# Kernel tuning notes

Measured on AMD Instinct MI355X. Metric: run time of the kernel, lower is better.

The kernel has to match this reference:

```python
import jax, jax.numpy as jnp
import numpy as np

T = 8
TAU = 2.0       # spikingjelly LIFNode default tau
VTH = 1.0       # default v_threshold
ALPHA = 2.0     # surrogate.ATan alpha
EPS = 1e-5      # BatchNorm eps


@jax.custom_vjp
def spike_fn(x):
    # Heaviside with ATan surrogate gradient
    return (x >= 0.0).astype(x.dtype)

def _spike_fwd(x):
    return (x >= 0.0).astype(x.dtype), x

def _spike_bwd(x, g):
    sg = (ALPHA / 2.0) / (1.0 + (jnp.pi / 2.0 * ALPHA * x) ** 2)
    return (g * sg,)

spike_fn.defvjp(_spike_fwd, _spike_bwd)


def lif(x_seq):
    """Multi-step LIF over leading time axis. decay_input=True, hard reset to 0, detach_reset."""
    def step(v, x):
        v = v + (x - v) / TAU            # charge
        s = spike_fn(v - VTH)            # fire (surrogate grad)
        v = v * (1.0 - jax.lax.stop_gradient(s))  # detached hard reset to v_reset=0
        return v, s
    _, s_seq = jax.lax.scan(step, jnp.zeros_like(x_seq[0]), x_seq)
    return s_seq


def conv2d(x, w, b, stride):
    y = jax.lax.conv_general_dilated(x, w, (stride, stride), 'VALID',
                                     dimension_numbers=('NCHW', 'OIHW', 'NCHW'))
    return y + b[None, :, None, None]


def batchnorm(x, g, b):
    # training-mode BN over merged (T*B, H, W) axes, matching step_mode='m' BatchNorm2d
    m = x.mean((0, 2, 3), keepdims=True)
    v = x.var((0, 2, 3), keepdims=True)
    return g[None, :, None, None] * (x - m) * jax.lax.rsqrt(v + EPS) + b[None, :, None, None]


def setup_inputs() -> dict:
    key = jax.random.key(0)
    ks = jax.random.split(key, 12)
    def w_init(k, shape):
        fan_in = int(np.prod(shape[1:]))
        return jax.random.normal(k, shape, dtype=jnp.float32) / np.sqrt(fan_in)
    x = jax.random.normal(ks[0], (128, 4, 84, 84), dtype=jnp.float32)
    return {
        'x': x,
        'conv1_w': w_init(ks[1], (32, 4, 8, 8)),  'conv1_b': jnp.zeros((32,), jnp.float32),
        'bn1_g': jnp.ones((32,), jnp.float32),    'bn1_b': jnp.zeros((32,), jnp.float32),
        'conv2_w': w_init(ks[2], (64, 32, 4, 4)), 'conv2_b': jnp.zeros((64,), jnp.float32),
        'bn2_g': jnp.ones((64,), jnp.float32),    'bn2_b': jnp.zeros((64,), jnp.float32),
        'conv3_w': w_init(ks[3], (64, 64, 3, 3)), 'conv3_b': jnp.zeros((64,), jnp.float32),
        'bn3_g': jnp.ones((64,), jnp.float32),    'bn3_b': jnp.zeros((64,), jnp.float32),
        'fc1_w': w_init(ks[4], (512, 3136)),      'fc1_b': jnp.zeros((512,), jnp.float32),
        'fco_w': w_init(ks[5], (2, 512)),         'fco_b': jnp.zeros((2,), jnp.float32),
    }


def reference(x, conv1_w, conv1_b, bn1_g, bn1_b, conv2_w, conv2_b, bn2_g, bn2_b,
              conv3_w, conv3_b, bn3_g, bn3_b, fc1_w, fc1_b, fco_w, fco_b):
    B = x.shape[0]
    # replicate input over T timesteps; fold T into batch for conv/BN (step_mode='m')
    xs = jnp.broadcast_to(x, (T,) + x.shape).reshape((T * B,) + x.shape[1:])

    h = batchnorm(conv2d(xs, conv1_w, conv1_b, 4), bn1_g, bn1_b)   # [TB,32,20,20]
    s = lif(h.reshape((T, B) + h.shape[1:]))
    h = s.reshape((T * B,) + s.shape[2:])

    h = batchnorm(conv2d(h, conv2_w, conv2_b, 2), bn2_g, bn2_b)    # [TB,64,9,9]
    s = lif(h.reshape((T, B) + h.shape[1:]))
    h = s.reshape((T * B,) + s.shape[2:])

    h = batchnorm(conv2d(h, conv3_w, conv3_b, 1), bn3_g, bn3_b)    # [TB,64,7,7]
    s = lif(h.reshape((T, B) + h.shape[1:]))                        # [T,B,64,7,7]

    feat = s.reshape(T, B, -1)                                      # [T,B,3136]
    hid = lif(jnp.einsum('tbi,oi->tbo', feat, fc1_w) + fc1_b)       # [T,B,512]
    out_seq = jnp.einsum('tbo,ko->tbk', hid, fco_w) + fco_b         # [T,B,2]
    return out_seq.mean(0)                                          # [B,2]
```

## Files before the change

kernel.cpp:

```cpp
#include <hip/hip_runtime.h>
#include <cstdint>
#include <cstddef>

#define TT 8

#define H1_ELEMS (128*32*20*20)
#define E2_ELEMS (128*64*81)
#define E3_ELEMS (128*64*49)

typedef __attribute__((ext_vector_type(8))) short short8;
typedef __attribute__((ext_vector_type(4))) float f32x4;

__global__ void prep_wT1(const float* __restrict__ w1, float* __restrict__ wT1) {
  int i = blockIdx.x * 256 + threadIdx.x;
  if (i >= 8192) return;
  int oc = i >> 8, pos = i & 255;
  wT1[(oc >> 4) * 4096 + pos * 16 + (oc & 15)] = w1[oc * 256 + pos];
}

__global__ void prep_w2frag(const float* __restrict__ w2, __bf16* __restrict__ wf) {
  int i = blockIdx.x * 256 + threadIdx.x;
  if (i >= 98304) return;
  int j    = i & 7;
  int oc   = (i >> 3) & 63;
  int quad = (i >> 9) & 3;
  int ksg  = (i >> 11) & 15;
  int term = i >> 15;
  int k = ksg * 32 + quad * 8 + j;
  int ci = k >> 4, kpos = k & 15;
  float w = w2[oc * 512 + ci * 16 + kpos];
  float hf = (float)(__bf16)w;
  float r1 = w - hf;
  float mf = (float)(__bf16)r1;
  float r2 = r1 - mf;
  __bf16 val = (term == 0) ? (__bf16)w : (term == 1) ? (__bf16)r1 : (__bf16)r2;
  wf[i] = val;
}

__global__ void prep_w3frag(const float* __restrict__ w3, __bf16* __restrict__ wf) {
  int i = blockIdx.x * 256 + threadIdx.x;
  if (i >= 110592) return;
  int j    = i & 7;
  int oc   = (i >> 3) & 63;
  int quad = (i >> 9) & 3;
  int tk   = i >> 11;
  int term = tk / 18, kstep = tk % 18;
  int k = kstep * 32 + quad * 8 + j;
  int pos = k >> 6, ci = k & 63;
  float w = w3[oc * 576 + ci * 9 + pos];
  float hf = (float)(__bf16)w;
  float r1 = w - hf;
  float mf = (float)(__bf16)r1;
  float r2 = r1 - mf;
  __bf16 val = (term == 0) ? (__bf16)w : (term == 1) ? (__bf16)r1 : (__bf16)r2;
  wf[i] = val;
}

__global__ void prep_wTf(const float* __restrict__ w, float* __restrict__ wT) {
  __shared__ float tile[32][33];
  int k0 = blockIdx.x * 32;
  int o0 = blockIdx.y * 32;
  int tx = threadIdx.x & 31, ty = threadIdx.x >> 5;
  #pragma unroll
  for (int j = 0; j < 4; j++)
    tile[ty + j * 8][tx] = w[(size_t)(o0 + ty + j * 8) * 3136 + k0 + tx];
  __syncthreads();
  #pragma unroll
  for (int j = 0; j < 4; j++)
    wT[(size_t)(k0 + ty + j * 8) * 512 + o0 + tx] = tile[tx][ty + j * 8];
}

__global__ __launch_bounds__(128) void k_conv1(const float* __restrict__ x,
                                               const float* __restrict__ wT,
                                               const float* __restrict__ bias,
                                               float* __restrict__ out) {
  __shared__ float xt[8064];
  int tid = threadIdx.x;
  int img = blockIdx.x >> 2;
  int q   = blockIdx.x & 3;
  int och = blockIdx.y;
  float4* dst = (float4*)xt;
  #pragma unroll
  for (int ci = 0; ci < 4; ci++) {
    const float4* s4 = (const float4*)(x + (size_t)img * 28224 + ci * 7056 + q * 1680);
    for (int i = tid; i < 504; i += 128) dst[ci * 504 + i] = s4[i];
  }
  __syncthreads();
  if (tid >= 100) return;
  int oyl = tid / 20, ox = tid % 20;
  float acc[16];
  #pragma unroll
  for (int j = 0; j < 16; j++) acc[j] = 0.f;
  int xb0 = oyl * 336 + ox * 4;
  const float* wh = wT + och * 4096;
  #pragma unroll 1
  for (int ci = 0; ci < 4; ci++) {
    #pragma unroll 1
    for (int ky = 0; ky < 8; ky++) {
      const float* xr = xt + ci * 2016 + xb0 + ky * 84;
      float4 xa  = *(const float4*)xr;
      float4 xbv = *(const float4*)(xr + 4);
      const float* wr = wh + (ci * 8 + ky) * 128;
      float xs[8] = {xa.x, xa.y, xa.z, xa.w, xbv.x, xbv.y, xbv.z, xbv.w};
      #pragma unroll
      for (int kx = 0; kx < 8; kx++) {
        #pragma unroll
        for (int j = 0; j < 16; j++)
          acc[j] = fmaf(xs[kx], wr[kx * 16 + j], acc[j]);
      }
    }
  }
  size_t obase = (size_t)img * 12800 + och * 6400 + (q * 5 + oyl) * 20 + ox;
  #pragma unroll
  for (int j = 0; j < 16; j++) out[obase + j * 400] = acc[j] + bias[och * 16 + j];
}

template <int HW>
__global__ void k_bnpartial(const float* __restrict__ xp, int C, int Nper,
                            float* __restrict__ pout) {
  int c = blockIdx.x, s = blockIdx.y, S = gridDim.y, tid = threadIdx.x;
  int n = Nper * HW;
  float sum = 0.f, sum2 = 0.f;
  for (int i = tid; i < n; i += 256) {
    int nb = s * Nper + i / HW;
    int p  = i % HW;
    float v = xp[((size_t)nb * C + c) * HW + p];
    sum += v; sum2 += v * v;
  }
  __shared__ float l0[256], l1[256];
  l0[tid] = sum; l1[tid] = sum2; __syncthreads();
  for (int k = 128; k > 0; k >>= 1) {
    if (tid < k) { l0[tid] += l0[tid + k]; l1[tid] += l1[tid + k]; }
    __syncthreads();
  }
  if (tid == 0) { pout[(c * S + s) * 2] = l0[0]; pout[(c * S + s) * 2 + 1] = l1[0]; }
}

__global__ void k_bnfinal(const float* __restrict__ pin, int S, float n,
                          float* __restrict__ meanArr, float* __restrict__ rstdArr) {
  int c = blockIdx.x, lane = threadIdx.x;
  float s = 0.f, s2 = 0.f;
  if (lane < S) { s = pin[(c * S + lane) * 2]; s2 = pin[(c * S + lane) * 2 + 1]; }
  for (int off = 8; off > 0; off >>= 1) { s += __shfl_down(s, off); s2 += __shfl_down(s2, off); }
  if (lane == 0) {
    float m = s / n;
    float var = s2 / n - m * m;
    meanArr[c] = m;
    rstdArr[c] = rsqrtf(var + 1e-5f);
  }
}

__global__ void k_lif1b(const float* __restrict__ h, const float* __restrict__ mean,
                        const float* __restrict__ rstd, const float* __restrict__ g,
                        const float* __restrict__ bb, uint32_t* __restrict__ sout) {
  int idx = blockIdx.x * 256 + threadIdx.x;
  int ic = idx / 20;
  int ci = ic & 31;
  const float* hp = h + (size_t)idx * 20;
  float gm = g[ci], mm = mean[ci], rs = rstd[ci], bc = bb[ci];
  float xv[20];
  #pragma unroll
  for (int j4 = 0; j4 < 5; j4++) {
    float4 hv = ((const float4*)hp)[j4];
    xv[j4 * 4 + 0] = gm * (hv.x - mm) * rs + bc;
    xv[j4 * 4 + 1] = gm * (hv.y - mm) * rs + bc;
    xv[j4 * 4 + 2] = gm * (hv.z - mm) * rs + bc;
    xv[j4 * 4 + 3] = gm * (hv.w - mm) * rs + bc;
  }
  float v[20];
  #pragma unroll
  for (int j = 0; j < 20; j++) v[j] = 0.f;
  #pragma unroll
  for (int t = 0; t < TT; t++) {
    uint32_t w = 0;
    #pragma unroll
    for (int j = 0; j < 20; j++) {
      v[j] = v[j] + (xv[j] - v[j]) * 0.5f;
      uint32_t s = (v[j] >= 1.0f);
      w |= s << j;
      if (s) v[j] = 0.f;
    }
    sout[t * 81920 + idx] = w;
  }
}

template <int W, int NROW>
__global__ void k_lifb(const float* __restrict__ h, const float* __restrict__ mean,
                       const float* __restrict__ rstd, const float* __restrict__ g,
                       const float* __restrict__ bb, uint32_t* __restrict__ sout,
                       int E) {
  int idx = blockIdx.x * 256 + threadIdx.x;
  int bc = idx / NROW;
  int c = bc & 63;
  float gm = g[c], mm = mean[c], rs = rstd[c], bcn = bb[c];
  float v[W];
  #pragma unroll
  for (int j = 0; j < W; j++) v[j] = 0.f;
  int nword = 128 * 64 * NROW;
  #pragma unroll
  for (int t = 0; t < TT; t++) {
    const float* hp = h + (size_t)t * E + (size_t)idx * W;
    uint32_t w = 0;
    #pragma unroll
    for (int j = 0; j < W; j++) {
      float xv = gm * (hp[j] - mm) * rs + bcn;
      v[j] = v[j] + (xv - v[j]) * 0.5f;
      uint32_t s = (v[j] >= 1.0f);
      w |= s << j;
      if (s) v[j] = 0.f;
    }
    sout[t * nword + idx] = w;
  }
}

__global__ __launch_bounds__(256) void k_conv2m(const uint32_t* __restrict__ s1b,
                                                const __bf16* __restrict__ wf,
                                                const float* __restrict__ bias,
                                                float* __restrict__ out) {
  __shared__ uint32_t sp[1280];
  __shared__ uint4 wl4[3072];
  __bf16* wl = (__bf16*)wl4;
  int tid = threadIdx.x;
  int img0 = blockIdx.x * 2;
  {
    const uint32_t* src = s1b + (size_t)img0 * 640;
    for (int i = tid; i < 1280; i += 256) sp[i] = src[i];
  }
  int wave = tid >> 6, lane = tid & 63;
  int img_local = wave >> 1;
  int tg = wave & 1;
  int l15 = lane & 15, quad = lane >> 4;
  int ci_off = quad >> 1;
  int kyp = (quad & 1) * 2;
  int spb[3], sh[3];
  #pragma unroll
  for (int mt = 0; mt < 3; mt++) {
    int px = tg * 48 + mt * 16 + l15;
    if (px > 80) px = 80;
    int oy = px / 9, ox = px - oy * 9;
    sh[mt]  = ox * 2;
    spb[mt] = img_local * 640 + ci_off * 20 + oy * 2 + kyp;
  }
  f32x4 acc[3][4];
  #pragma unroll
  for (int mt = 0; mt < 3; mt++)
    #pragma unroll
    for (int nt = 0; nt < 4; nt++) acc[mt][nt] = (f32x4){0.f, 0.f, 0.f, 0.f};

  for (int kc = 0; kc < 4; kc++) {
    __syncthreads();
    for (int o = tid * 8; o < 24576; o += 2048) {
      int tk = o >> 11;
      int term = tk >> 2, ksl = tk & 3;
      const __bf16* src = wf + (((term * 16 + kc * 4 + ksl)) << 11) + (o & 2047);
      *(uint4*)(wl + o) = *(const uint4*)src;
    }
    __syncthreads();
    #pragma unroll
    for (int ks = 0; ks < 4; ks++) {
      int ksg = kc * 4 + ks;
      short8 a[3];
      #pragma unroll
      for (int mt = 0; mt < 3; mt++) {
        uint32_t w0 = sp[spb[mt] + ksg * 40];
        uint32_t w1 = sp[spb[mt] + ksg * 40 + 1];
        uint32_t n0 = (w0 >> sh[mt]) & 15u;
        uint32_t n1 = (w1 >> sh[mt]) & 15u;
        union { uint32_t u[4]; short8 v; } A;
        A.u[0] = ((n0 & 1u) ? 0x3F80u : 0u) | ((n0 & 2u) ? 0x3F800000u : 0u);
        A.u[1] = ((n0 & 4u) ? 0x3F80u : 0u) | ((n0 & 8u) ? 0x3F800000u : 0u);
        A.u[2] = ((n1 & 1u) ? 0x3F80u : 0u) | ((n1 & 2u) ? 0x3F800000u : 0u);
        A.u[3] = ((n1 & 4u) ? 0x3F80u : 0u) | ((n1 & 8u) ? 0x3F800000u : 0u);
        a[mt] = A.v;
      }
      #pragma unroll
      for (int term = 0; term < 3; term++) {
        int fb = ((term * 4 + ks) << 11) + (quad << 9);
        #pragma unroll
        for (int nt = 0; nt < 4; nt++) {
          short8 b = *(const short8*)(wl + fb + ((nt << 4) + l15) * 8);
          #pragma unroll
          for (int mt = 0; mt < 3; mt++)
            acc[mt][nt] = __builtin_amdgcn_mfma_f32_16x16x32_bf16(a[mt], b, acc[mt][nt], 0, 0, 0);
        }
      }
    }
  }
  #pragma unroll
  for (int nt = 0; nt < 4; nt++) {
    int oc = nt * 16 + l15;
    float bv = bias[oc];
    float* op = out + ((size_t)(img0 + img_local) * 64 + oc) * 81;
    #pragma unroll
    for (int mt = 0; mt < 3; mt++) {
      int pxr = tg * 48 + mt * 16 + quad * 4;
      #pragma unroll
      for (int r = 0; r < 4; r++) {
        int px = pxr + r;
        if (px < 81) op[px] = acc[mt][nt][r] + bv;
      }
    }
  }
}

__global__ void k_s2T(const uint32_t* __restrict__ sbits, uint32_t* __restrict__ s2T) {
  __shared__ uint32_t sb[576];
  int n = blockIdx.x;
  int t = n >> 7, b = n & 127;
  int tid = threadIdx.x;
  const uint32_t* src = sbits + t * 73728 + b * 576;
  for (int i = tid; i < 576; i += 256) sb[i] = src[i];
  __syncthreads();
  if (tid >= 162) return;
  int half = tid & 1, pc = tid >> 1;
  int r = pc / 9, cpix = pc - r * 9;
  uint32_t w = 0;
  #pragma unroll
  for (int ci = 0; ci < 32; ci++)
    w |= (((sb[(half * 32 + ci) * 9 + r] >> cpix) & 1u) << ci);
  s2T[(size_t)n * 162 + pc * 2 + half] = w;
}

__global__ __launch_bounds__(256) void k_conv3m(const uint32_t* __restrict__ s2T,
                                                const __bf16* __restrict__ wf,
                                                const float* __restrict__ bias,
                                                float* __restrict__ out) {
  __shared__ uint32_t sp[324];
  __shared__ uint4 wl4[4608];
  __bf16* wl = (__bf16*)wl4;
  int tid = threadIdx.x;
  int img0 = blockIdx.x * 2;
  {
    const uint32_t* src = s2T + (size_t)img0 * 162;
    for (int i = tid; i < 324; i += 256) sp[i] = src[i];
  }
  int wave = tid >> 6, lane = tid & 63;
  int img_local = wave >> 1, tg = wave & 1;
  int l15 = lane & 15, quad = lane >> 4;
  int qsh = quad * 8;
  int base[2];
  #pragma unroll
  for (int mt = 0; mt < 2; mt++) {
    int px = tg * 32 + mt * 16 + l15;
    if (px > 48) px = 48;
    int oy = px / 7, ox = px - oy * 7;
    base[mt] = img_local * 162 + (oy * 9 + ox) * 2;
  }
  f32x4 acc[2][4];
  #pragma unroll
  for (int mt = 0; mt < 2; mt++)
    #pragma unroll
    for (int nt = 0; nt < 4; nt++) acc[mt][nt] = (f32x4){0.f, 0.f, 0.f, 0.f};

  #pragma unroll
  for (int kc = 0; kc < 3; kc++) {
    __syncthreads();
    #pragma unroll
    for (int it = 0; it < 18; it++) {
      const __bf16* s = wf + (((it / 6) * 18 + kc * 6 + (it % 6)) << 11) + tid * 8;
      *(uint4*)(wl + (it << 11) + tid * 8) = *(const uint4*)s;
    }
    __syncthreads();
    #pragma unroll
    for (int ksl = 0; ksl < 6; ksl++) {
      int kstep = kc * 6 + ksl;
      int pos = kstep >> 1, cihalf = kstep & 1;
      int ky = pos / 3, kx = pos % 3;
      short8 a[2];
      #pragma unroll
      for (int mt = 0; mt < 2; mt++) {
        uint32_t word = sp[base[mt] + (ky * 9 + kx) * 2 + cihalf];
        uint32_t byt = (word >> qsh) & 255u;
        union { uint32_t u[4]; short8 v; } A;
        A.u[0] = ((byt & 1u)  ? 0x3F80u : 0u) | ((byt & 2u)   ? 0x3F800000u : 0u);
        A.u[1] = ((byt & 4u)  ? 0x3F80u : 0u) | ((byt & 8u)   ? 0x3F800000u : 0u);
        A.u[2] = ((byt & 16u) ? 0x3F80u : 0u) | ((byt & 32u)  ? 0x3F800000u : 0u);
        A.u[3] = ((byt & 64u) ? 0x3F80u : 0u) | ((byt & 128u) ? 0x3F800000u : 0u);
        a[mt] = A.v;
      }
      #pragma unroll
      for (int term = 0; term < 3; term++) {
        int fb = ((term * 6 + ksl) << 11) + (quad << 9);
        #pragma unroll
        for (int nt = 0; nt < 4; nt++) {
          short8 b = *(const short8*)(wl + fb + ((nt << 4) + l15) * 8);
          #pragma unroll
          for (int mt = 0; mt < 2; mt++)
            acc[mt][nt] = __builtin_amdgcn_mfma_f32_16x16x32_bf16(a[mt], b, acc[mt][nt], 0, 0, 0);
        }
      }
    }
  }
  #pragma unroll
  for (int nt = 0; nt < 4; nt++) {
    int oc = nt * 16 + l15;
    float bv = bias[oc];
    float* op = out + ((size_t)(img0 + img_local) * 64 + oc) * 49;
    #pragma unroll
    for (int mt = 0; mt < 2; mt++) {
      int pxr = tg * 32 + mt * 16 + quad * 4;
      #pragma unroll
      for (int r = 0; r < 4; r++) {
        int px = pxr + r;
        if (px < 49) op[px] = acc[mt][nt][r] + bv;
      }
    }
  }
}

__global__ __launch_bounds__(256) void k_fc1(const uint32_t* __restrict__ s3b,
                                             const float* __restrict__ wT,
                                             float* __restrict__ part) {
  __shared__ float xs[16 * 196];
  int tid = threadIdx.x;
  int rowblk = blockIdx.x >> 4;
  int kc     = blockIdx.x & 15;
  int row0 = rowblk * 16;
  int kb   = kc * 196;
  for (int i = tid; i < 448; i += 256) {
    int r = i / 28, rem = i - r * 28;
    int c = rem / 7, row = rem - c * 7;
    uint32_t w = s3b[(size_t)(row0 + r) * 448 + (kc * 4 + c) * 7 + row];
    int base = r * 196 + c * 49 + row * 7;
    #pragma unroll
    for (int xq = 0; xq < 7; xq++)
      xs[base + xq] = (float)((w >> xq) & 1u);
  }
  __syncthreads();
  int oc2 = tid * 2;
  float2 acc[16];
  #pragma unroll
  for (int r = 0; r < 16; r++) { acc[r].x = 0.f; acc[r].y = 0.f; }
  const float* wp = wT + (size_t)kb * 512 + oc2;
  const float4* xs4 = (const float4*)xs;
  for (int k4 = 0; k4 < 49; k4++) {
    float2 w0 = *(const float2*)(wp + (size_t)(k4 * 4 + 0) * 512);
    float2 w1 = *(const float2*)(wp + (size_t)(k4 * 4 + 1) * 512);
    float2 w2 = *(const float2*)(wp + (size_t)(k4 * 4 + 2) * 512);
    float2 w3 = *(const float2*)(wp + (size_t)(k4 * 4 + 3) * 512);
    #pragma unroll
    for (int r = 0; r < 16; r++) {
      float4 xv = xs4[r * 49 + k4];
      acc[r].x = fmaf(xv.x, w0.x, acc[r].x);  acc[r].y = fmaf(xv.x, w0.y, acc[r].y);
      acc[r].x = fmaf(xv.y, w1.x, acc[r].x);  acc[r].y = fmaf(xv.y, w1.y, acc[r].y);
      acc[r].x = fmaf(xv.z, w2.x, acc[r].x);  acc[r].y = fmaf(xv.z, w2.y, acc[r].y);
      acc[r].x = fmaf(xv.w, w3.x, acc[r].x);  acc[r].y = fmaf(xv.w, w3.y, acc[r].y);
    }
  }
  #pragma unroll
  for (int r = 0; r < 16; r++) {
    float* o = part + (size_t)kc * 524288 + (size_t)(row0 + r) * 512 + oc2;
    o[0] = acc[r].x; o[1] = acc[r].y;
  }
}

__global__ void k_fc1red_lif(const float* __restrict__ part, const float* __restrict__ bias,
                             unsigned char* __restrict__ hid) {
  int idx = blockIdx.x * 256 + threadIdx.x;
  float bv = bias[idx & 511];
  float v = 0.f;
  #pragma unroll
  for (int t = 0; t < TT; t++) {
    float a = part[t * 65536 + idx];
    #pragma unroll
    for (int j = 1; j < 16; j++) a += part[(size_t)j * 524288 + t * 65536 + idx];
    a += bv;
    v = v + (a - v) * 0.5f;
    unsigned char s = (v >= 1.0f);
    hid[t * 65536 + idx] = s;
    if (s) v = 0.f;
  }
}

__global__ void k_fco(const unsigned char* __restrict__ hid, const float* __restrict__ w,
                      const float* __restrict__ bias, float* __restrict__ out) {
  int b = blockIdx.x, tid = threadIdx.x;
  float a0 = 0.f, a1 = 0.f;
  for (int t = 0; t < TT; t++) {
    const unsigned char* hrow = hid + ((size_t)t * 128 + b) * 512;
    for (int o = tid; o < 512; o += 256) {
      if (hrow[o]) { a0 += w[o]; a1 += w[512 + o]; }
    }
  }
  __shared__ float l0[256], l1[256];
  l0[tid] = a0; l1[tid] = a1; __syncthreads();
  for (int k = 128; k > 0; k >>= 1) {
    if (tid < k) { l0[tid] += l0[tid + k]; l1[tid] += l1[tid + k]; }
    __syncthreads();
  }
  if (tid == 0) {
    out[b * 2 + 0] = l0[0] * 0.125f + bias[0];
    out[b * 2 + 1] = l1[0] * 0.125f + bias[1];
  }
}

extern "C" void kernel_launch(void* const* d_in, const int* in_sizes, int n_in,
                              void* d_out, int out_size, void* d_ws, size_t ws_size,
                              hipStream_t stream) {
  const float* x    = (const float*)d_in[0];
  const float* c1w  = (const float*)d_in[1];
  const float* c1b  = (const float*)d_in[2];
  const float* bn1g = (const float*)d_in[3];
  const float* bn1b = (const float*)d_in[4];
  const float* c2w  = (const float*)d_in[5];
  const float* c2b  = (const float*)d_in[6];
  const float* bn2g = (const float*)d_in[7];
  const float* bn2b = (const float*)d_in[8];
  const float* c3w  = (const float*)d_in[9];
  const float* c3b  = (const float*)d_in[10];
  const float* bn3g = (const float*)d_in[11];
  const float* bn3b = (const float*)d_in[12];
  const float* fc1w = (const float*)d_in[13];
  const float* fc1b = (const float*)d_in[14];
  const float* fcow = (const float*)d_in[15];
  const float* fcob = (const float*)d_in[16];
  float* out = (float*)d_out;

  char* ws = (char*)d_ws;
  float*    h1     = (float*)(ws + 0);
  uint32_t* s1bits = (uint32_t*)(ws + 6553600);
  float*    h2     = (float*)(ws + 19660800);
  uint32_t* s2bits = (uint32_t*)(ws + 40894464);
  float*    h3     = (float*)(ws + 46202880);
  uint32_t* s3bits = (uint32_t*)(ws + 59047936);
  unsigned char* hid = (unsigned char*)(ws + 64356352);
  float*    st     = (float*)(ws + 64880640);
  __bf16*   w2f  = (__bf16*)(ws + 60882944);
  __bf16*   w3f  = (__bf16*)(ws + 61079552);
  uint32_t* s2T  = (uint32_t*)(ws + 61300736);
  float*    wT1  = (float*)(ws + 62390272);
  float* wTf    = (float*)(ws + 0);
  float* bnpart = (float*)(ws + 9437184);
  float* f1part = (float*)(ws + 19660800);

  prep_wT1   <<<32, 256, 0, stream>>>(c1w, wT1);
  prep_w2frag<<<384, 256, 0, stream>>>(c2w, w2f);
  prep_w3frag<<<432, 256, 0, stream>>>(c3w, w3f);
  k_conv1    <<<dim3(512, 2), 128, 0, stream>>>(x, wT1, c1b, h1);
  k_bnpartial<400><<<dim3(32, 16), 256, 0, stream>>>(h1, 32, 8, bnpart);
  k_bnfinal  <<<32, 64, 0, stream>>>(bnpart, 16, 128.f * 400.f, st, st + 32);
  k_lif1b    <<<320, 256, 0, stream>>>(h1, st, st + 32, bn1g, bn1b, s1bits);
  prep_wTf   <<<dim3(98, 16), 256, 0, stream>>>(fc1w, wTf);

  k_conv2m   <<<512, 256, 0, stream>>>(s1bits, w2f, c2b, h2);
  k_bnpartial<81><<<dim3(64, 16), 256, 0, stream>>>(h2, 64, 64, bnpart);
  k_bnfinal  <<<64, 64, 0, stream>>>(bnpart, 16, 1024.f * 81.f, st + 64, st + 128);
  k_lifb<9, 9><<<288, 256, 0, stream>>>(h2, st + 64, st + 128, bn2g, bn2b, s2bits, E2_ELEMS);

  k_s2T      <<<1024, 256, 0, stream>>>(s2bits, s2T);
  k_conv3m   <<<512, 256, 0, stream>>>(s2T, w3f, c3b, h3);
  k_bnpartial<49><<<dim3(64, 16), 256, 0, stream>>>(h3, 64, 64, bnpart);
  k_bnfinal  <<<64, 64, 0, stream>>>(bnpart, 16, 1024.f * 49.f, st + 192, st + 256);
  k_lifb<7, 7><<<224, 256, 0, stream>>>(h3, st + 192, st + 256, bn3g, bn3b, s3bits, E3_ELEMS);

  k_fc1      <<<1024, 256, 0, stream>>>(s3bits, wTf, f1part);
  k_fc1red_lif<<<256, 256, 0, stream>>>(f1part, fc1b, hid);
  k_fco      <<<128, 256, 0, stream>>>(hid, fcow, fcob, out);
}
```

Measured before the change: 286.0 us.

## Move fc1 to bf16 MFMA with 3-term split weights and bit-packed spikes

```diff
diff --git a/kernel.cpp b/kernel.cpp
--- a/kernel.cpp
+++ b/kernel.cpp
@@ -56,18 +56,27 @@
   wf[i] = val;
 }
 
-__global__ void prep_wTf(const float* __restrict__ w, float* __restrict__ wT) {
-  __shared__ float tile[32][33];
-  int k0 = blockIdx.x * 32;
-  int o0 = blockIdx.y * 32;
-  int tx = threadIdx.x & 31, ty = threadIdx.x >> 5;
-  #pragma unroll
-  for (int j = 0; j < 4; j++)
-    tile[ty + j * 8][tx] = w[(size_t)(o0 + ty + j * 8) * 3136 + k0 + tx];
-  __syncthreads();
-  #pragma unroll
-  for (int j = 0; j < 4; j++)
-    wT[(size_t)(k0 + ty + j * 8) * 512 + o0 + tx] = tile[tx][ty + j * 8];
+__global__ void prep_wff(const float* __restrict__ w, __bf16* __restrict__ wf) {
+  int i = blockIdx.x * 256 + threadIdx.x;
+  if (i >= 602112) return;
+  int oc   = i & 511;
+  int quad = (i >> 9) & 3;
+  int ts   = i >> 11;
+  int term = ts / 98, s = ts - term * 98;
+  int kbase = s * 32 + quad * 8;
+  int pos = kbase >> 6;
+  int ci0 = kbase & 63;
+  union { __bf16 h[8]; short8 v; } V;
+  #pragma unroll
+  for (int j = 0; j < 8; j++) {
+    float wv = w[(size_t)oc * 3136 + (ci0 + j) * 49 + pos];
+    float hf = (float)(__bf16)wv;
+    float r1 = wv - hf;
+    float mf = (float)(__bf16)r1;
+    float r2 = r1 - mf;
+    V.h[j] = (term == 0) ? (__bf16)wv : (term == 1) ? (__bf16)r1 : (__bf16)r2;
+  }
+  *(short8*)(wf + (size_t)i * 8) = V.v;
 }
 
 __global__ __launch_bounds__(128) void k_conv1(const float* __restrict__ x,
@@ -408,49 +417,87 @@
   }
 }
 
-__global__ __launch_bounds__(256) void k_fc1(const uint32_t* __restrict__ s3b,
-                                             const float* __restrict__ wT,
-                                             float* __restrict__ part) {
-  __shared__ float xs[16 * 196];
+__global__ void k_s3T(const uint32_t* __restrict__ sbits, uint32_t* __restrict__ s3T) {
+  __shared__ uint32_t sb[896];
+  int r0 = blockIdx.x * 2;
   int tid = threadIdx.x;
-  int rowblk = blockIdx.x >> 4;
-  int kc     = blockIdx.x & 15;
-  int row0 = rowblk * 16;
-  int kb   = kc * 196;
-  for (int i = tid; i < 448; i += 256) {
-    int r = i / 28, rem = i - r * 28;
-    int c = rem / 7, row = rem - c * 7;
-    uint32_t w = s3b[(size_t)(row0 + r) * 448 + (kc * 4 + c) * 7 + row];
-    int base = r * 196 + c * 49 + row * 7;
-    #pragma unroll
-    for (int xq = 0; xq < 7; xq++)
-      xs[base + xq] = (float)((w >> xq) & 1u);
+  for (int i = tid; i < 896; i += 256) {
+    int rl = i / 448, o = i - rl * 448;
+    int row = r0 + rl;
+    sb[i] = sbits[(row >> 7) * 57344 + (row & 127) * 448 + o];
   }
   __syncthreads();
-  int oc2 = tid * 2;
-  float2 acc[16];
-  #pragma unroll
-  for (int r = 0; r < 16; r++) { acc[r].x = 0.f; acc[r].y = 0.f; }
-  const float* wp = wT + (size_t)kb * 512 + oc2;
-  const float4* xs4 = (const float4*)xs;
-  for (int k4 = 0; k4 < 49; k4++) {
-    float2 w0 = *(const float2*)(wp + (size_t)(k4 * 4 + 0) * 512);
-    float2 w1 = *(const float2*)(wp + (size_t)(k4 * 4 + 1) * 512);
-    float2 w2 = *(const float2*)(wp + (size_t)(k4 * 4 + 2) * 512);
-    float2 w3 = *(const float2*)(wp + (size_t)(k4 * 4 + 3) * 512);
-    #pragma unroll
-    for (int r = 0; r < 16; r++) {
-      float4 xv = xs4[r * 49 + k4];
-      acc[r].x = fmaf(xv.x, w0.x, acc[r].x);  acc[r].y = fmaf(xv.x, w0.y, acc[r].y);
-      acc[r].x = fmaf(xv.y, w1.x, acc[r].x);  acc[r].y = fmaf(xv.y, w1.y, acc[r].y);
-      acc[r].x = fmaf(xv.z, w2.x, acc[r].x);  acc[r].y = fmaf(xv.z, w2.y, acc[r].y);
-      acc[r].x = fmaf(xv.w, w3.x, acc[r].x);  acc[r].y = fmaf(xv.w, w3.y, acc[r].y);
-    }
-  }
-  #pragma unroll
-  for (int r = 0; r < 16; r++) {
-    float* o = part + (size_t)kc * 524288 + (size_t)(row0 + r) * 512 + oc2;
-    o[0] = acc[r].x; o[1] = acc[r].y;
+  if (tid >= 196) return;
+  int rl = tid / 98, k = tid - rl * 98;
+  int pos = k >> 1, half = k & 1;
+  int py = pos / 7, px = pos - py * 7;
+  const uint32_t* base = sb + rl * 448 + half * 224 + py;
+  uint32_t w = 0;
+  #pragma unroll
+  for (int ci = 0; ci < 32; ci++)
+    w |= ((base[ci * 7] >> px) & 1u) << ci;
+  s3T[(size_t)(r0 + rl) * 98 + k] = w;
+}
+
+__global__ __launch_bounds__(256) void k_fc1m(const uint32_t* __restrict__ s3T,
+                                              const __bf16* __restrict__ wf,
+                                              float* __restrict__ part) {
+  __shared__ uint32_t aS[6272];
+  int tid = threadIdx.x;
+  int row0 = blockIdx.x * 64;
+  int oc0  = blockIdx.y * 32;
+  {
+    const uint32_t* src = s3T + (size_t)row0 * 98;
+    for (int i = tid; i < 6272; i += 256) aS[i] = src[i];
+  }
+  __syncthreads();
+  int wave = tid >> 6, lane = tid & 63;
+  int l15 = lane & 15, quad = lane >> 4;
+  int qsh = quad * 8;
+  f32x4 acc[4][2];
+  #pragma unroll
+  for (int mt = 0; mt < 4; mt++)
+    #pragma unroll
+    for (int nt = 0; nt < 2; nt++) acc[mt][nt] = (f32x4){0.f, 0.f, 0.f, 0.f};
+  int nIter = (wave < 2) ? 25 : 24;
+  #pragma unroll 1
+  for (int i = 0; i < nIter; i++) {
+    int ks = i * 4 + wave;
+    short8 a[4];
+    #pragma unroll
+    for (int mt = 0; mt < 4; mt++) {
+      uint32_t word = aS[(mt * 16 + l15) * 98 + ks];
+      uint32_t byt = (word >> qsh) & 255u;
+      union { uint32_t u[4]; short8 v; } A;
+      A.u[0] = ((byt & 1u)  ? 0x3F80u : 0u) | ((byt & 2u)   ? 0x3F800000u : 0u);
+      A.u[1] = ((byt & 4u)  ? 0x3F80u : 0u) | ((byt & 8u)   ? 0x3F800000u : 0u);
+      A.u[2] = ((byt & 16u) ? 0x3F80u : 0u) | ((byt & 32u)  ? 0x3F800000u : 0u);
+      A.u[3] = ((byt & 64u) ? 0x3F80u : 0u) | ((byt & 128u) ? 0x3F800000u : 0u);
+      a[mt] = A.v;
+    }
+    #pragma unroll
+    for (int term = 0; term < 3; term++) {
+      size_t fb = ((size_t)((term * 98 + ks) * 4 + quad) * 512 + oc0 + l15) * 8;
+      #pragma unroll
+      for (int nt = 0; nt < 2; nt++) {
+        short8 b = *(const short8*)(wf + fb + nt * 128);
+        #pragma unroll
+        for (int mt = 0; mt < 4; mt++)
+          acc[mt][nt] = __builtin_amdgcn_mfma_f32_16x16x32_bf16(a[mt], b, acc[mt][nt], 0, 0, 0);
+      }
+    }
+  }
+  #pragma unroll
+  for (int mt = 0; mt < 4; mt++) {
+    #pragma unroll
+    for (int nt = 0; nt < 2; nt++) {
+      int oc = oc0 + nt * 16 + l15;
+      #pragma unroll
+      for (int r = 0; r < 4; r++) {
+        int row = row0 + mt * 16 + quad * 4 + r;
+        part[(size_t)wave * 524288 + (size_t)row * 512 + oc] = acc[mt][nt][r];
+      }
+    }
   }
 }
 
@@ -463,7 +510,7 @@
   for (int t = 0; t < TT; t++) {
     float a = part[t * 65536 + idx];
     #pragma unroll
-    for (int j = 1; j < 16; j++) a += part[(size_t)j * 524288 + t * 65536 + idx];
+    for (int j = 1; j < 4; j++) a += part[(size_t)j * 524288 + t * 65536 + idx];
     a += bv;
     v = v + (a - v) * 0.5f;
     unsigned char s = (v >= 1.0f);
@@ -529,9 +576,10 @@
   __bf16*   w3f  = (__bf16*)(ws + 61079552);
   uint32_t* s2T  = (uint32_t*)(ws + 61300736);
   float*    wT1  = (float*)(ws + 62390272);
-  float* wTf    = (float*)(ws + 0);
-  float* bnpart = (float*)(ws + 9437184);
-  float* f1part = (float*)(ws + 19660800);
+  float*    bnpart = (float*)(ws + 9437184);
+  __bf16*   wff    = (__bf16*)(ws + 19660800);
+  float*    f1part = (float*)(ws + 29360128);
+  uint32_t* s3T    = (uint32_t*)(ws + 43253760);
 
   prep_wT1   <<<32, 256, 0, stream>>>(c1w, wT1);
   prep_w2frag<<<384, 256, 0, stream>>>(c2w, w2f);
@@ -540,12 +588,12 @@
   k_bnpartial<400><<<dim3(32, 16), 256, 0, stream>>>(h1, 32, 8, bnpart);
   k_bnfinal  <<<32, 64, 0, stream>>>(bnpart, 16, 128.f * 400.f, st, st + 32);
   k_lif1b    <<<320, 256, 0, stream>>>(h1, st, st + 32, bn1g, bn1b, s1bits);
-  prep_wTf   <<<dim3(98, 16), 256, 0, stream>>>(fc1w, wTf);
 
   k_conv2m   <<<512, 256, 0, stream>>>(s1bits, w2f, c2b, h2);
   k_bnpartial<81><<<dim3(64, 16), 256, 0, stream>>>(h2, 64, 64, bnpart);
   k_bnfinal  <<<64, 64, 0, stream>>>(bnpart, 16, 1024.f * 81.f, st + 64, st + 128);
   k_lifb<9, 9><<<288, 256, 0, stream>>>(h2, st + 64, st + 128, bn2g, bn2b, s2bits, E2_ELEMS);
+  prep_wff   <<<2352, 256, 0, stream>>>(fc1w, wff);
 
   k_s2T      <<<1024, 256, 0, stream>>>(s2bits, s2T);
   k_conv3m   <<<512, 256, 0, stream>>>(s2T, w3f, c3b, h3);
@@ -553,7 +601,8 @@
   k_bnfinal  <<<64, 64, 0, stream>>>(bnpart, 16, 1024.f * 49.f, st + 192, st + 256);
   k_lifb<7, 7><<<224, 256, 0, stream>>>(h3, st + 192, st + 256, bn3g, bn3b, s3bits, E3_ELEMS);
 
-  k_fc1      <<<1024, 256, 0, stream>>>(s3bits, wTf, f1part);
+  k_s3T      <<<512, 256, 0, stream>>>(s3bits, s3T);
+  k_fc1m     <<<dim3(16, 16), 256, 0, stream>>>(s3T, wff, f1part);
   k_fc1red_lif<<<256, 256, 0, stream>>>(f1part, fc1b, hid);
   k_fco      <<<128, 256, 0, stream>>>(hid, fcow, fcob, out);
 }
```

Result: no change. 288.9 us (+1.0%).
